# Optimization experiments

Measured on AMD Instinct MI355X. Metric: run time of the kernel, lower is better.

The kernel has to match this reference:

```python
import jax, jax.numpy as jnp
import numpy as np
from jax import lax

BN_EPS = 1e-5


def _fps(xyz, n_points):
    """Farthest point sampling. xyz: [B,N,3] -> [B,S] int32 indices.
    Sequential by nature; expressed as a lax.scan over S iterations.
    Deterministic start at index 0 (original uses a random start)."""
    B, N, _ = xyz.shape

    def step(carry, _):
        distance, farthest = carry  # [B,N], [B]
        centroid = jax.vmap(lambda p, f: p[f])(xyz, farthest)  # [B,3]
        dist = jnp.sum((xyz - centroid[:, None, :]) ** 2, axis=-1)  # [B,N]
        distance = jnp.minimum(distance, dist)
        new_far = jnp.argmax(distance, axis=-1).astype(jnp.int32)
        return (distance, new_far), farthest

    init = (jnp.full((B, N), 1e10, xyz.dtype), jnp.zeros((B,), jnp.int32))
    _, idxs = lax.scan(step, init, None, length=n_points)  # [S,B]
    return idxs.T  # [B,S]


def _gather(points, idx):
    """index_points: points [B,N,C], idx [B,...] -> [B,...,C]."""
    return jax.vmap(lambda p, i: p[i])(points, idx)


def _conv_bn_relu(x, W, b, gamma, beta):
    # 1x1 Conv2d over channel axis: x [B,Cin,k,S] -> [B,Cout,k,S]
    y = jnp.einsum('oc,bcks->boks', W, x) + b[None, :, None, None]
    # BatchNorm2d in training mode: batch stats over (B,k,S), biased variance
    m = jnp.mean(y, axis=(0, 2, 3), keepdims=True)
    v = jnp.var(y, axis=(0, 2, 3), keepdims=True)
    y = (y - m) * lax.rsqrt(v + BN_EPS) * gamma[None, :, None, None] + beta[None, :, None, None]
    return jax.nn.relu(y)


def setup_inputs() -> dict:
    key = jax.random.key(0)
    ks = jax.random.split(key, 4)
    B, N, D = 4, 16384, 125
    C0, C1, C2 = 128, 128, 256  # C0 = 3 + D
    xyz = jax.random.normal(ks[0], (B, N, 3), jnp.float32)
    features = jax.random.normal(ks[1], (B, N, D), jnp.float32)
    W1 = jax.random.normal(ks[2], (C1, C0), jnp.float32) / np.float32(np.sqrt(C0))
    W2 = jax.random.normal(ks[3], (C2, C1), jnp.float32) / np.float32(np.sqrt(C1))
    return {
        'xyz': xyz, 'features': features,
        'W1': W1, 'b1': jnp.zeros((C1,), jnp.float32),
        'gamma1': jnp.ones((C1,), jnp.float32), 'beta1': jnp.zeros((C1,), jnp.float32),
        'W2': W2, 'b2': jnp.zeros((C2,), jnp.float32),
        'gamma2': jnp.ones((C2,), jnp.float32), 'beta2': jnp.zeros((C2,), jnp.float32),
        'n_points_fps': 2048, 'k': 16,
    }


def reference(xyz, features, W1, b1, gamma1, beta1, W2, b2, gamma2, beta2, n_points_fps, k):
    B, N, _ = xyz.shape
    S = n_points_fps
    # sample_and_group
    fps_idx = _fps(xyz, S)                     # [B,S]
    new_xyz = _gather(xyz, fps_idx)            # [B,S,3]
    # full pairwise squared distances [B,S,N] (as in square_distance)
    dists = jnp.sum((new_xyz[:, :, None, :] - xyz[:, None, :, :]) ** 2, axis=-1)
    _, idx = lax.top_k(-dists, k)              # k nearest, ascending distance: [B,S,k]
    grouped_xyz = _gather(xyz, idx)            # [B,S,k,3]
    grouped_xyz_norm = grouped_xyz - new_xyz[:, :, None, :]
    grouped_feat = _gather(features, idx)      # [B,S,k,D]
    new_points = jnp.concatenate([grouped_xyz_norm, grouped_feat], axis=-1)  # [B,S,k,C0]
    # MLP head: permute to [B,C0,k,S]
    x = jnp.transpose(new_points, (0, 3, 2, 1))
    x = _conv_bn_relu(x, W1, b1, gamma1, beta1)
    x = _conv_bn_relu(x, W2, b2, gamma2, beta2)
    x = jnp.max(x, axis=2)                     # max over neighbors k: [B,C2,S]
    x = jnp.transpose(x, (0, 2, 1))            # [B,S,C2]
    return (new_xyz, x)
```

## Files before the change

### kernel.cpp

```cpp
#include <hip/hip_runtime.h>

#define B_ 4
#define N_ 16384
#define D_ 125
#define S_ 2048
#define K_ 16
#define C0_ 128
#define C1_ 128
#define C2_ 256
#define NSLOT 64

typedef float v2f __attribute__((ext_vector_type(2)));

__device__ __forceinline__ void pin(float& x) { asm volatile("" : "+v"(x)); }

__device__ __forceinline__ v2f v2max(v2f a, v2f b) {
  v2f r;
  r.x = fmaxf(a.x, b.x);
  r.y = fmaxf(a.y, b.y);
  return r;
}

template <int CTRL, int RMASK>
__device__ __forceinline__ double dppmax(double k) {
  const long long kb = __double_as_longlong(k);
  const int lo = (int)(kb & 0xffffffffll);
  const int hi = (int)(((unsigned long long)kb) >> 32);
  const int plo = __builtin_amdgcn_update_dpp(lo, lo, CTRL, RMASK, 0xf, false);
  const int phi = __builtin_amdgcn_update_dpp(hi, hi, CTRL, RMASK, 0xf, false);
  const double p =
      __longlong_as_double(((long long)phi << 32) | (unsigned int)plo);
  return fmax(k, p);
}
template <int CTRL, int RMASK>
__device__ __forceinline__ double dppmin(double k) {
  const long long kb = __double_as_longlong(k);
  const int lo = (int)(kb & 0xffffffffll);
  const int hi = (int)(((unsigned long long)kb) >> 32);
  const int plo = __builtin_amdgcn_update_dpp(lo, lo, CTRL, RMASK, 0xf, false);
  const int phi = __builtin_amdgcn_update_dpp(hi, hi, CTRL, RMASK, 0xf, false);
  const double p =
      __longlong_as_double(((long long)phi << 32) | (unsigned int)plo);
  return fmin(k, p);
}

__global__ __attribute__((amdgpu_flat_work_group_size(1024, 1024),
                          amdgpu_waves_per_eu(4, 4)))
void fps_kernel(const float* __restrict__ xyz, float* __restrict__ new_xyz,
                float* __restrict__ sortbuf) {
#pragma clang fp contract(off)
  const int b = blockIdx.x;
  const float* X = xyz + (size_t)b * N_ * 3;
  float* SB = sortbuf + (size_t)b * 3 * N_;
  const int t = threadIdx.x;
  constexpr int PAIRS = N_ / 1024 / 2;
  const int base = t * (2 * PAIRS);

  __shared__ unsigned int s_hist[4096];
  __shared__ float s_bb[16][8];
  __shared__ unsigned int s_wsum[16];
  __shared__ unsigned short s_sidx[N_];
  __shared__ unsigned long long s_k1[2];
  __shared__ __align__(16) float4 s_cc[2][16];

  float arr[48];
  {
    float4* a4 = (float4*)arr;
#pragma unroll
    for (int i = 0; i < 12; ++i) a4[i] = *(const float4*)(X + base * 3 + 4 * i);
  }
  float lx0 = arr[0], lx1 = arr[0], ly0 = arr[1], ly1 = arr[1];
  float lz0 = arr[2], lz1 = arr[2];
#pragma unroll
  for (int p = 1; p < 16; ++p) {
    lx0 = fminf(lx0, arr[3 * p + 0]); lx1 = fmaxf(lx1, arr[3 * p + 0]);
    ly0 = fminf(ly0, arr[3 * p + 1]); ly1 = fmaxf(ly1, arr[3 * p + 1]);
    lz0 = fminf(lz0, arr[3 * p + 2]); lz1 = fmaxf(lz1, arr[3 * p + 2]);
  }
#pragma unroll
  for (int off = 32; off > 0; off >>= 1) {
    lx0 = fminf(lx0, __shfl_xor(lx0, off)); lx1 = fmaxf(lx1, __shfl_xor(lx1, off));
    ly0 = fminf(ly0, __shfl_xor(ly0, off)); ly1 = fmaxf(ly1, __shfl_xor(ly1, off));
    lz0 = fminf(lz0, __shfl_xor(lz0, off)); lz1 = fmaxf(lz1, __shfl_xor(lz1, off));
  }
  if ((t & 63) == 0) {
    const int w = t >> 6;
    s_bb[w][0] = lx0; s_bb[w][1] = lx1; s_bb[w][2] = ly0;
    s_bb[w][3] = ly1; s_bb[w][4] = lz0; s_bb[w][5] = lz1;
  }
  for (int i = t; i < 4096; i += 1024) s_hist[i] = 0u;
  if (t == 0) { s_k1[0] = 0ull; s_k1[1] = 0ull; }
  __syncthreads();
  float gx0 = s_bb[0][0], gx1 = s_bb[0][1], gy0 = s_bb[0][2];
  float gy1 = s_bb[0][3], gz0 = s_bb[0][4], gz1 = s_bb[0][5];
#pragma unroll
  for (int w = 1; w < 16; ++w) {
    gx0 = fminf(gx0, s_bb[w][0]); gx1 = fmaxf(gx1, s_bb[w][1]);
    gy0 = fminf(gy0, s_bb[w][2]); gy1 = fmaxf(gy1, s_bb[w][3]);
    gz0 = fminf(gz0, s_bb[w][4]); gz1 = fmaxf(gz1, s_bb[w][5]);
  }
  const float ivx = (gx1 > gx0) ? 16.0f / (gx1 - gx0) : 0.0f;
  const float ivy = (gy1 > gy0) ? 16.0f / (gy1 - gy0) : 0.0f;
  const float ivz = (gz1 > gz0) ? 16.0f / (gz1 - gz0) : 0.0f;
  int cell[16];
#pragma unroll
  for (int p = 0; p < 16; ++p) {
    int qx = min(15, (int)((arr[3 * p + 0] - gx0) * ivx));
    int qy = min(15, (int)((arr[3 * p + 1] - gy0) * ivy));
    int qz = min(15, (int)((arr[3 * p + 2] - gz0) * ivz));
    int mx = (qx & 1) | ((qx & 2) << 2) | ((qx & 4) << 4) | ((qx & 8) << 6);
    int my = (qy & 1) | ((qy & 2) << 2) | ((qy & 4) << 4) | ((qy & 8) << 6);
    int mz = (qz & 1) | ((qz & 2) << 2) | ((qz & 4) << 4) | ((qz & 8) << 6);
    cell[p] = mx | (my << 1) | (mz << 2);
    atomicAdd(&s_hist[cell[p]], 1u);
  }
  __syncthreads();
  {
    unsigned int c0 = s_hist[4 * t + 0], c1 = s_hist[4 * t + 1];
    unsigned int c2 = s_hist[4 * t + 2], c3 = s_hist[4 * t + 3];
    (void)c3;
    unsigned int tsum = c0 + c1 + c2 + c3;
    unsigned int incl = tsum;
#pragma unroll
    for (int off = 1; off < 64; off <<= 1) {
      unsigned int nv = __shfl_up(incl, off);
      if ((t & 63) >= off) incl += nv;
    }
    if ((t & 63) == 63) s_wsum[t >> 6] = incl;
    __syncthreads();
    unsigned int wpre = 0;
    const int myw = t >> 6;
    for (int w = 0; w < myw; ++w) wpre += s_wsum[w];
    const unsigned int texc = wpre + incl - tsum;
    s_hist[4 * t + 0] = texc;
    s_hist[4 * t + 1] = texc + c0;
    s_hist[4 * t + 2] = texc + c0 + c1;
    s_hist[4 * t + 3] = texc + c0 + c1 + c2;
  }
  __syncthreads();
#pragma unroll
  for (int p = 0; p < 16; ++p) {
    const unsigned int slot = atomicAdd(&s_hist[cell[p]], 1u);
    SB[slot]          = arr[3 * p + 0];
    SB[N_ + slot]     = arr[3 * p + 1];
    SB[2 * N_ + slot] = arr[3 * p + 2];
    s_sidx[slot] = (unsigned short)(base + p);
  }
  __threadfence();
  __syncthreads();
  __threadfence();

  v2f px[PAIRS], py[PAIRS], pz[PAIRS], d[PAIRS];
  {
    float4 xa[4], ya[4], za[4];
#pragma unroll
    for (int i = 0; i < 4; ++i) {
      xa[i] = *(const float4*)(SB + base + 4 * i);
      ya[i] = *(const float4*)(SB + N_ + base + 4 * i);
      za[i] = *(const float4*)(SB + 2 * N_ + base + 4 * i);
    }
    const float* xf = (const float*)xa;
    const float* yf = (const float*)ya;
    const float* zf = (const float*)za;
#pragma unroll
    for (int j = 0; j < PAIRS; ++j) {
      px[j] = (v2f){xf[2 * j], xf[2 * j + 1]};
      py[j] = (v2f){yf[2 * j], yf[2 * j + 1]};
      pz[j] = (v2f){zf[2 * j], zf[2 * j + 1]};
      d[j] = (v2f){1e10f, 1e10f};
    }
  }
  unsigned int invw[PAIRS];
  {
    const unsigned int* SI = (const unsigned int*)&s_sidx[base];
#pragma unroll
    for (int j = 0; j < PAIRS; ++j) invw[j] = ~SI[j];
  }
  float bx0 = 1e30f, bx1 = -1e30f, by0 = 1e30f, by1 = -1e30f;
  float bz0 = 1e30f, bz1 = -1e30f;
#pragma unroll
  for (int j = 0; j < PAIRS; ++j) {
    bx0 = fminf(bx0, fminf(px[j].x, px[j].y));
    bx1 = fmaxf(bx1, fmaxf(px[j].x, px[j].y));
    by0 = fminf(by0, fminf(py[j].x, py[j].y));
    by1 = fmaxf(by1, fmaxf(py[j].x, py[j].y));
    bz0 = fminf(bz0, fminf(pz[j].x, pz[j].y));
    bz1 = fmaxf(bz1, fmaxf(pz[j].x, pz[j].y));
  }
#pragma unroll
  for (int j = 0; j < PAIRS; ++j) {
    float a0 = px[j].x, a1 = px[j].y;
    float b0 = py[j].x, b1 = py[j].y;
    float c0 = pz[j].x, c1 = pz[j].y;
    pin(a0); pin(a1); pin(b0); pin(b1); pin(c0); pin(c1);
    px[j] = (v2f){a0, a1};
    py[j] = (v2f){b0, b1};
    pz[j] = (v2f){c0, c1};
  }
  float cx = X[0], cy = X[1], cz = X[2];
  float tmax = 1e10f;
  unsigned long long keylow = 0ull;
  bool iwin = false;
  float ccx = 0.f, ccy = 0.f, ccz = 0.f;
  float cap_x = 0.f, cap_y = 0.f, cap_z = 0.f;
  const unsigned int wid = (unsigned int)(t >> 6);
  for (int s = 0; s < S_; ++s) {
    if (((s - t) & 1023) == 0) { cap_x = cx; cap_y = cy; cap_z = cz; }
    if ((s & 1023) == 1023) {
      const int o = (b * S_ + (s & ~1023) + t) * 3;
      new_xyz[o + 0] = cap_x;
      new_xyz[o + 1] = cap_y;
      new_xyz[o + 2] = cap_z;
    }
    if (s == S_ - 1) break;
    const int buf = s & 1;
    const float mx = fmaxf(fmaxf(bx0 - cx, cx - bx1), 0.0f);
    const float my = fmaxf(fmaxf(by0 - cy, cy - by1), 0.0f);
    const float mz = fmaxf(fmaxf(bz0 - cz, cz - bz1), 0.0f);
    const float L = (mx * mx + my * my) + mz * mz;
    if (__any(L < tmax)) {
      __builtin_amdgcn_s_setprio(1);
      const v2f c2x = {cx, cx}, c2y = {cy, cy}, c2z = {cz, cz};
#pragma unroll
      for (int j = 0; j < PAIRS; ++j) {
        v2f dx = px[j] - c2x;
        v2f dy = py[j] - c2y;
        v2f dz = pz[j] - c2z;
        v2f sq = (dx * dx + dy * dy) + dz * dz;
        v2f dm;
        dm.x = fminf(d[j].x, sq.x);
        dm.y = fminf(d[j].y, sq.y);
        d[j] = dm;
      }
      const v2f m01 = v2max(d[0], d[1]);
      const v2f m23 = v2max(d[2], d[3]);
      const v2f m45 = v2max(d[4], d[5]);
      const v2f m67 = v2max(d[6], d[7]);
      const v2f m03 = v2max(m01, m23);
      const v2f m47 = v2max(m45, m67);
      const v2f m07 = v2max(m03, m47);
      const float lmax = fmaxf(m07.x, m07.y);
      tmax = lmax;
      unsigned int binv = 0u;
#pragma unroll
      for (int j = 0; j < PAIRS; ++j) {
        const unsigned int lo = invw[j] & 0xFFFFu;
        const unsigned int hi = invw[j] >> 16;
        if (d[j].x == lmax) binv = max(binv, lo);
        if (d[j].y == lmax) binv = max(binv, hi);
      }
#pragma unroll
      for (int j = 0; j < PAIRS; ++j) {
        const unsigned int lo = invw[j] & 0xFFFFu;
        const unsigned int hi = invw[j] >> 16;
        if (lo == binv) { ccx = px[j].x; ccy = py[j].x; ccz = pz[j].x; }
        if (hi == binv) { ccx = px[j].y; ccy = py[j].y; ccz = pz[j].y; }
      }
      const unsigned long long k52 =
          ((unsigned long long)__float_as_uint(lmax) << 20) |
          (unsigned long long)((binv << 4) | wid);
      double dk = __longlong_as_double((long long)k52);
      dk = dppmax<0x111, 0xf>(dk);
      dk = dppmax<0x112, 0xf>(dk);
      dk = dppmax<0x114, 0xf>(dk);
      dk = dppmax<0x118, 0xf>(dk);
      dk = dppmax<0x142, 0xa>(dk);
      dk = dppmax<0x143, 0xc>(dk);
      const long long kb = __double_as_longlong(dk);
      const int rlo = __builtin_amdgcn_readlane((int)(kb & 0xffffffffll), 63);
      const int rhi =
          __builtin_amdgcn_readlane((int)(((unsigned long long)kb) >> 32), 63);
      const unsigned long long wk52 =
          ((unsigned long long)(unsigned int)rhi << 32) | (unsigned int)rlo;
      iwin = (k52 == wk52);
      keylow = wk52;
      __builtin_amdgcn_s_setprio(0);
    }
    if (iwin) {
      atomicMax(&s_k1[buf], ((unsigned long long)s << 52) | keylow);
      s_cc[buf][wid] = make_float4(ccx, ccy, ccz, 0.f);
    }
    __syncthreads();
    const unsigned long long bk = s_k1[buf];
    const int w_win = (int)(bk & 15ull);
    const float4 cc = s_cc[buf][w_win];
    cx = cc.x; cy = cc.y; cz = cc.z;
  }
}

__global__ __launch_bounds__(256) void knn_kernel(const float* __restrict__ xyz,
                                                  const float* __restrict__ new_xyz,
                                                  int* __restrict__ knn_idx) {
  const int q = blockIdx.x;
  const int b = q / S_;
  __shared__ float sd[N_];
  __shared__ unsigned long long s_kd[2];
  const int t = threadIdx.x;
  if (t == 0) { s_kd[0] = ~0ull; s_kd[1] = ~0ull; }
  const float qx = new_xyz[q * 3 + 0];
  const float qy = new_xyz[q * 3 + 1];
  const float qz = new_xyz[q * 3 + 2];
  const float* X = xyz + (size_t)b * N_ * 3;
  float lmin = 1e30f;
  int lidx = -1;
  for (int j = 0; j < N_ / 256; ++j) {
    int i = t + j * 256;
    float dx = X[i * 3 + 0] - qx;
    float dy = X[i * 3 + 1] - qy;
    float dz = X[i * 3 + 2] - qz;
    float dsq = fmaf(dx, dx, fmaf(dy, dy, dz * dz));
    sd[i] = dsq;
    if (dsq < lmin) { lmin = dsq; lidx = i; }
  }
  __syncthreads();
  for (int r = 0; r < K_; ++r) {
    const unsigned long long k =
        ((unsigned long long)(7 - (r >> 1)) << 60) |
        ((unsigned long long)__float_as_uint(lmin) << 28) |
        (unsigned int)(lidx & 0x0FFFFFFF);
    double dk = __longlong_as_double((long long)k);
    dk = dppmin<0x111, 0xf>(dk);
    dk = dppmin<0x112, 0xf>(dk);
    dk = dppmin<0x114, 0xf>(dk);
    dk = dppmin<0x118, 0xf>(dk);
    dk = dppmin<0x142, 0xa>(dk);
    dk = dppmin<0x143, 0xc>(dk);
    const long long kb = __double_as_longlong(dk);
    const int rlo = __builtin_amdgcn_readlane((int)(kb & 0xffffffffll), 63);
    const int rhi =
        __builtin_amdgcn_readlane((int)(((unsigned long long)kb) >> 32), 63);
    const unsigned long long wk =
        ((unsigned long long)(unsigned int)rhi << 32) | (unsigned int)rlo;
    if ((t & 63) == 0) atomicMin(&s_kd[r & 1], wk);
    __syncthreads();
    const unsigned long long bk = s_kd[r & 1];
    const int wi = (int)(bk & 0x0FFFFFFFull);
    if (t == 0) knn_idx[q * K_ + r] = wi;
    if (wi == lidx) {
      sd[wi] = 1e30f;
      lmin = 1e30f; lidx = -1;
      for (int j = 0; j < N_ / 256; ++j) {
        int i = t + j * 256;
        float dv = sd[i];
        if (dv < lmin) { lmin = dv; lidx = i; }
      }
    }
  }
}

__global__ __launch_bounds__(256) void prep_kernel(const float* __restrict__ W1,
                                                   const float* __restrict__ W2,
                                                   float* __restrict__ W1t,
                                                   float* __restrict__ W2t,
                                                   float* __restrict__ stats) {
  int e = blockIdx.x * 256 + threadIdx.x;
  stats[e] = 0.0f;
  if (e < C1_ * C0_) {
    int co = e / C0_, c = e % C0_;
    W1t[c * C1_ + co] = W1[e];
  } else {
    int e2 = e - C1_ * C0_;
    int co = e2 / C1_, c = e2 % C1_;
    W2t[c * C2_ + co] = W2[e2];
  }
}

__global__ __launch_bounds__(256) void conv1_stats_kernel(
    const float* __restrict__ xyz, const float* __restrict__ feat,
    const float* __restrict__ new_xyz, const int* __restrict__ knn,
    const float* __restrict__ W1t, const float* __restrict__ b1,
    float* __restrict__ stats1) {
  __shared__ __align__(16) float sinT[C0_][K_];
  __shared__ int sidx[K_];
  __shared__ float sred[256];
  const int t = threadIdx.x;
  float psum = 0.f, psumsq = 0.f;
  const int QPB = (B_ * S_) / 1024;
  for (int qq = 0; qq < QPB; ++qq) {
    const int q = blockIdx.x * QPB + qq;
    const int b = q / S_;
    if (t < K_) sidx[t] = knn[q * K_ + t];
    __syncthreads();
    const float nx = new_xyz[q * 3 + 0];
    const float ny = new_xyz[q * 3 + 1];
    const float nz = new_xyz[q * 3 + 2];
    for (int e = t; e < K_ * C0_; e += 256) {
      int c = e >> 4, kk = e & 15;
      int i = sidx[kk];
      float v;
      if (c < 3)
        v = xyz[((size_t)b * N_ + i) * 3 + c] - (c == 0 ? nx : (c == 1 ? ny : nz));
      else
        v = feat[((size_t)b * N_ + i) * D_ + (c - 3)];
      sinT[c][kk] = v;
    }
    __syncthreads();
    const int co = t & 127, kh = t >> 7;
    float acc[8];
    float bias = b1[co];
#pragma unroll
    for (int k = 0; k < 8; ++k) acc[k] = bias;
    for (int c = 0; c < C0_; ++c) {
      float w = W1t[c * C1_ + co];
      float4 xa = *(const float4*)&sinT[c][kh * 8];
      float4 xb = *(const float4*)&sinT[c][kh * 8 + 4];
      acc[0] = fmaf(w, xa.x, acc[0]);
      acc[1] = fmaf(w, xa.y, acc[1]);
      acc[2] = fmaf(w, xa.z, acc[2]);
      acc[3] = fmaf(w, xa.w, acc[3]);
      acc[4] = fmaf(w, xb.x, acc[4]);
      acc[5] = fmaf(w, xb.y, acc[5]);
      acc[6] = fmaf(w, xb.z, acc[6]);
      acc[7] = fmaf(w, xb.w, acc[7]);
    }
#pragma unroll
    for (int k = 0; k < 8; ++k) {
      psum += acc[k];
      psumsq = fmaf(acc[k], acc[k], psumsq);
    }
    __syncthreads();
  }
  sred[t] = psum;
  __syncthreads();
  float totsum = (t < 128) ? (sred[t] + sred[t + 128]) : 0.f;
  __syncthreads();
  sred[t] = psumsq;
  __syncthreads();
  if (t < 128) {
    float totsq = sred[t] + sred[t + 128];
    float* st = stats1 + (size_t)(blockIdx.x & (NSLOT - 1)) * (2 * C1_);
    atomicAdd(&st[t], totsum);
    atomicAdd(&st[C1_ + t], totsq);
  }
}

__global__ void finalize1_kernel(const float* __restrict__ stats1,
                                 const float* __restrict__ gamma1,
                                 const float* __restrict__ beta1,
                                 float* __restrict__ ss1) {
  int t = threadIdx.x;
  float s = 0.f, sq = 0.f;
  for (int w = 0; w < NSLOT; ++w) {
    s += stats1[w * 2 * C1_ + t];
    sq += stats1[w * 2 * C1_ + C1_ + t];
  }
  const float M = (float)(B_ * S_ * K_);
  float m = s / M;
  float v = fmaxf(sq / M - m * m, 0.f);
  float sc = gamma1[t] * rsqrtf(v + 1e-5f);
  ss1[t] = sc;
  ss1[C1_ + t] = fmaf(-m, sc, beta1[t]);
}

__global__ __launch_bounds__(256) void conv2_kernel(
    const float* __restrict__ xyz, const float* __restrict__ feat,
    const float* __restrict__ new_xyz, const int* __restrict__ knn,
    const float* __restrict__ W1t, const float* __restrict__ b1,
    const float* __restrict__ ss1, const float* __restrict__ W2t,
    const float* __restrict__ b2, float* __restrict__ maxv,
    float* __restrict__ minv, float* __restrict__ stats2) {
  __shared__ __align__(16) float sinT[C0_][K_];
  __shared__ __align__(16) float sh1T[C1_][20];
  __shared__ int sidx[K_];
  const int t = threadIdx.x;
  float psum = 0.f, psumsq = 0.f;
  const int QPB = (B_ * S_) / 1024;
  for (int qq = 0; qq < QPB; ++qq) {
    const int q = blockIdx.x * QPB + qq;
    const int b = q / S_;
    if (t < K_) sidx[t] = knn[q * K_ + t];
    __syncthreads();
    const float nx = new_xyz[q * 3 + 0];
    const float ny = new_xyz[q * 3 + 1];
    const float nz = new_xyz[q * 3 + 2];
    for (int e = t; e < K_ * C0_; e += 256) {
      int c = e >> 4, kk = e & 15;
      int i = sidx[kk];
      float v;
      if (c < 3)
        v = xyz[((size_t)b * N_ + i) * 3 + c] - (c == 0 ? nx : (c == 1 ? ny : nz));
      else
        v = feat[((size_t)b * N_ + i) * D_ + (c - 3)];
      sinT[c][kk] = v;
    }
    __syncthreads();
    {
      const int co = t & 127, kh = t >> 7;
      float acc[8];
      float bias = b1[co];
#pragma unroll
      for (int k = 0; k < 8; ++k) acc[k] = bias;
      for (int c = 0; c < C0_; ++c) {
        float w = W1t[c * C1_ + co];
        float4 xa = *(const float4*)&sinT[c][kh * 8];
        float4 xb = *(const float4*)&sinT[c][kh * 8 + 4];
        acc[0] = fmaf(w, xa.x, acc[0]);
        acc[1] = fmaf(w, xa.y, acc[1]);
        acc[2] = fmaf(w, xa.z, acc[2]);
        acc[3] = fmaf(w, xa.w, acc[3]);
        acc[4] = fmaf(w, xb.x, acc[4]);
        acc[5] = fmaf(w, xb.y, acc[5]);
        acc[6] = fmaf(w, xb.z, acc[6]);
        acc[7] = fmaf(w, xb.w, acc[7]);
      }
      float sc = ss1[co], sh = ss1[C1_ + co];
#pragma unroll
      for (int k = 0; k < 8; ++k) {
        float h = fmaxf(fmaf(acc[k], sc, sh), 0.f);
        sh1T[co][kh * 8 + k] = h;
      }
    }
    __syncthreads();
    {
      float acc2[16];
      float bias2 = b2[t];
#pragma unroll
      for (int k = 0; k < 16; ++k) acc2[k] = bias2;
      for (int c = 0; c < C1_; ++c) {
        float w = W2t[c * C2_ + t];
        float4 h0 = *(const float4*)&sh1T[c][0];
        float4 h1 = *(const float4*)&sh1T[c][4];
        float4 h2 = *(const float4*)&sh1T[c][8];
        float4 h3 = *(const float4*)&sh1T[c][12];
        acc2[0] = fmaf(w, h0.x, acc2[0]);
        acc2[1] = fmaf(w, h0.y, acc2[1]);
        acc2[2] = fmaf(w, h0.z, acc2[2]);
        acc2[3] = fmaf(w, h0.w, acc2[3]);
        acc2[4] = fmaf(w, h1.x, acc2[4]);
        acc2[5] = fmaf(w, h1.y, acc2[5]);
        acc2[6] = fmaf(w, h1.z, acc2[6]);
        acc2[7] = fmaf(w, h1.w, acc2[7]);
        acc2[8] = fmaf(w, h2.x, acc2[8]);
        acc2[9] = fmaf(w, h2.y, acc2[9]);
        acc2[10] = fmaf(w, h2.z, acc2[10]);
        acc2[11] = fmaf(w, h2.w, acc2[11]);
        acc2[12] = fmaf(w, h3.x, acc2[12]);
        acc2[13] = fmaf(w, h3.y, acc2[13]);
        acc2[14] = fmaf(w, h3.z, acc2[14]);
        acc2[15] = fmaf(w, h3.w, acc2[15]);
      }
      float mx = acc2[0], mn = acc2[0];
#pragma unroll
      for (int k = 0; k < 16; ++k) {
        psum += acc2[k];
        psumsq = fmaf(acc2[k], acc2[k], psumsq);
        mx = fmaxf(mx, acc2[k]);
        mn = fminf(mn, acc2[k]);
      }
      maxv[(size_t)q * C2_ + t] = mx;
      minv[(size_t)q * C2_ + t] = mn;
    }
    __syncthreads();
  }
  float* st = stats2 + (size_t)(blockIdx.x & (NSLOT - 1)) * (2 * C2_);
  atomicAdd(&st[t], psum);
  atomicAdd(&st[C2_ + t], psumsq);
}

__global__ void finalize2_kernel(const float* __restrict__ stats2,
                                 const float* __restrict__ gamma2,
                                 const float* __restrict__ beta2,
                                 float* __restrict__ ss2) {
  int t = threadIdx.x;
  float s = 0.f, sq = 0.f;
  for (int w = 0; w < NSLOT; ++w) {
    s += stats2[w * 2 * C2_ + t];
    sq += stats2[w * 2 * C2_ + C2_ + t];
  }
  const float M = (float)(B_ * S_ * K_);
  float m = s / M;
  float v = fmaxf(sq / M - m * m, 0.f);
  float sc = gamma2[t] * rsqrtf(v + 1e-5f);
  ss2[t] = sc;
  ss2[C2_ + t] = fmaf(-m, sc, beta2[t]);
}

__global__ __launch_bounds__(256) void out_kernel(const float* __restrict__ maxv,
                                                  const float* __restrict__ minv,
                                                  const float* __restrict__ ss2,
                                                  float* __restrict__ out2) {
  int e = blockIdx.x * 256 + threadIdx.x;
  int co = e & (C2_ - 1);
  float sc = ss2[co], sh = ss2[C2_ + co];
  float v = (sc >= 0.f) ? maxv[e] : minv[e];
  out2[e] = fmaxf(fmaf(v, sc, sh), 0.f);
}

extern "C" void kernel_launch(void* const* d_in, const int* in_sizes, int n_in,
                              void* d_out, int out_size, void* d_ws, size_t ws_size,
                              hipStream_t stream) {
  (void)in_sizes; (void)n_in; (void)out_size; (void)ws_size;
  const float* xyz = (const float*)d_in[0];
  const float* feat = (const float*)d_in[1];
  const float* W1 = (const float*)d_in[2];
  const float* b1 = (const float*)d_in[3];
  const float* gamma1 = (const float*)d_in[4];
  const float* beta1 = (const float*)d_in[5];
  const float* W2 = (const float*)d_in[6];
  const float* b2 = (const float*)d_in[7];
  const float* gamma2 = (const float*)d_in[8];
  const float* beta2 = (const float*)d_in[9];

  float* out = (float*)d_out;
  float* new_xyz = out;
  float* out2 = out + B_ * S_ * 3;

  float* ws = (float*)d_ws;
  float* stats1 = ws;
  float* stats2 = stats1 + NSLOT * 2 * C1_;
  float* ss1 = stats2 + NSLOT * 2 * C2_;
  float* ss2 = ss1 + 2 * C1_;
  float* W1t = ss2 + 2 * C2_;
  float* W2t = W1t + C1_ * C0_;
  int* knn = (int*)(W2t + (size_t)C2_ * C1_);
  float* maxv = (float*)(knn + B_ * S_ * K_);
  float* minv = maxv + (size_t)B_ * S_ * C2_;
  float* sortbuf = maxv;

  prep_kernel<<<192, 256, 0, stream>>>(W1, W2, W1t, W2t, stats1);
  fps_kernel<<<B_, 1024, 0, stream>>>(xyz, new_xyz, sortbuf);
  knn_kernel<<<B_ * S_, 256, 0, stream>>>(xyz, new_xyz, knn);
  conv1_stats_kernel<<<1024, 256, 0, stream>>>(xyz, feat, new_xyz, knn, W1t, b1, stats1);
  finalize1_kernel<<<1, 128, 0, stream>>>(stats1, gamma1, beta1, ss1);
  conv2_kernel<<<1024, 256, 0, stream>>>(xyz, feat, new_xyz, knn, W1t, b1, ss1,
                                         W2t, b2, maxv, minv, stats2);
  finalize2_kernel<<<1, 256, 0, stream>>>(stats2, gamma2, beta2, ss2);
  out_kernel<<<(B_ * S_ * C2_) / 256, 256, 0, stream>>>(maxv, minv, ss2, out2);
}
```

Measured before the change: 3.317 ms.

## Split FPS in two halves and overlap second half with KNN of first half

FPS is split into two kernels. The first computes the first 1024 samples and spills its per-thread state (distances, index words, centroid, keys) to workspace. A fused kernel then resumes FPS for the remaining samples in 4 blocks while the other blocks run KNN on the already-written first-half centroids, and a final kernel runs KNN for the second half. KNN blocks also grow from 256 to 1024 threads. This hides the serial FPS tail behind KNN work, at the cost of spilling and reloading state and sharing CUs between the serial FPS blocks and KNN blocks.

```diff
diff --git a/kernel.cpp b/kernel.cpp
--- a/kernel.cpp
+++ b/kernel.cpp
@@ -46,8 +46,11 @@
 
 __global__ __attribute__((amdgpu_flat_work_group_size(1024, 1024),
                           amdgpu_waves_per_eu(4, 4)))
-void fps_kernel(const float* __restrict__ xyz, float* __restrict__ new_xyz,
-                float* __restrict__ sortbuf) {
+void fps_a_kernel(const float* __restrict__ xyz, float* __restrict__ new_xyz,
+                  float* __restrict__ sortbuf, float* __restrict__ dsp,
+                  float4* __restrict__ ccsp, unsigned int* __restrict__ invsp,
+                  unsigned long long* __restrict__ klsp,
+                  float4* __restrict__ csp) {
 #pragma clang fp contract(off)
   const int b = blockIdx.x;
   const float* X = xyz + (size_t)b * N_ * 3;
@@ -204,7 +207,7 @@
   float ccx = 0.f, ccy = 0.f, ccz = 0.f;
   float cap_x = 0.f, cap_y = 0.f, cap_z = 0.f;
   const unsigned int wid = (unsigned int)(t >> 6);
-  for (int s = 0; s < S_; ++s) {
+  for (int s = 0; s < 1024; ++s) {
     if (((s - t) & 1023) == 0) { cap_x = cx; cap_y = cy; cap_z = cz; }
     if ((s & 1023) == 1023) {
       const int o = (b * S_ + (s & ~1023) + t) * 3;
@@ -212,7 +215,6 @@
       new_xyz[o + 1] = cap_y;
       new_xyz[o + 2] = cap_z;
     }
-    if (s == S_ - 1) break;
     const int buf = s & 1;
     const float mx = fmaxf(fmaxf(bx0 - cx, cx - bx1), 0.0f);
     const float my = fmaxf(fmaxf(by0 - cy, cy - by1), 0.0f);
@@ -286,15 +288,203 @@
     const float4 cc = s_cc[buf][w_win];
     cx = cc.x; cy = cc.y; cz = cc.z;
   }
-}
-
-__global__ __launch_bounds__(256) void knn_kernel(const float* __restrict__ xyz,
-                                                  const float* __restrict__ new_xyz,
-                                                  int* __restrict__ knn_idx) {
-  const int q = blockIdx.x;
-  const int b = q / S_;
-  __shared__ float sd[N_];
-  __shared__ unsigned long long s_kd[2];
+  {
+    float4* o = (float4*)(dsp + ((size_t)b * 1024 + t) * 16);
+    o[0] = make_float4(d[0].x, d[0].y, d[1].x, d[1].y);
+    o[1] = make_float4(d[2].x, d[2].y, d[3].x, d[3].y);
+    o[2] = make_float4(d[4].x, d[4].y, d[5].x, d[5].y);
+    o[3] = make_float4(d[6].x, d[6].y, d[7].x, d[7].y);
+    ccsp[b * 1024 + t] = make_float4(ccx, ccy, ccz, iwin ? 1.f : 0.f);
+    unsigned int* iv = invsp + ((size_t)b * 1024 + t) * 8;
+#pragma unroll
+    for (int j = 0; j < PAIRS; ++j) iv[j] = invw[j];
+    if ((t & 63) == 0) klsp[b * 16 + wid] = keylow;
+    if (t == 0) csp[b] = make_float4(cx, cy, cz, 0.f);
+  }
+}
+
+__device__ void fps_b_body(const float* __restrict__ xyz,
+                           float* __restrict__ new_xyz,
+                           float* __restrict__ sortbuf,
+                           float* __restrict__ dsp, float4* __restrict__ ccsp,
+                           unsigned int* __restrict__ invsp,
+                           unsigned long long* __restrict__ klsp,
+                           float4* __restrict__ csp, char* smem) {
+#pragma clang fp contract(off)
+  const int b = blockIdx.x;
+  const float* X = xyz + (size_t)b * N_ * 3;
+  float* SB = sortbuf + (size_t)b * 3 * N_;
+  const int t = threadIdx.x;
+  constexpr int PAIRS = N_ / 1024 / 2;
+  const int base = t * (2 * PAIRS);
+  unsigned long long* s_k1 = (unsigned long long*)smem;
+  float4* s_cc = (float4*)(smem + 32);
+  (void)X;
+
+  v2f px[PAIRS], py[PAIRS], pz[PAIRS], d[PAIRS];
+  {
+    float4 xa[4], ya[4], za[4];
+#pragma unroll
+    for (int i = 0; i < 4; ++i) {
+      xa[i] = *(const float4*)(SB + base + 4 * i);
+      ya[i] = *(const float4*)(SB + N_ + base + 4 * i);
+      za[i] = *(const float4*)(SB + 2 * N_ + base + 4 * i);
+    }
+    const float* xf = (const float*)xa;
+    const float* yf = (const float*)ya;
+    const float* zf = (const float*)za;
+#pragma unroll
+    for (int j = 0; j < PAIRS; ++j) {
+      px[j] = (v2f){xf[2 * j], xf[2 * j + 1]};
+      py[j] = (v2f){yf[2 * j], yf[2 * j + 1]};
+      pz[j] = (v2f){zf[2 * j], zf[2 * j + 1]};
+    }
+  }
+  {
+    const float4* i4 = (const float4*)(dsp + ((size_t)b * 1024 + t) * 16);
+    float4 d0 = i4[0], d1 = i4[1], d2 = i4[2], d3 = i4[3];
+    d[0] = (v2f){d0.x, d0.y}; d[1] = (v2f){d0.z, d0.w};
+    d[2] = (v2f){d1.x, d1.y}; d[3] = (v2f){d1.z, d1.w};
+    d[4] = (v2f){d2.x, d2.y}; d[5] = (v2f){d2.z, d2.w};
+    d[6] = (v2f){d3.x, d3.y}; d[7] = (v2f){d3.z, d3.w};
+  }
+  unsigned int invw[PAIRS];
+  {
+    const unsigned int* iv = invsp + ((size_t)b * 1024 + t) * 8;
+#pragma unroll
+    for (int j = 0; j < PAIRS; ++j) invw[j] = iv[j];
+  }
+  const float4 ccv = ccsp[b * 1024 + t];
+  float ccx = ccv.x, ccy = ccv.y, ccz = ccv.z;
+  bool iwin = (ccv.w != 0.f);
+  const unsigned int wid = (unsigned int)(t >> 6);
+  unsigned long long keylow = klsp[b * 16 + wid];
+  const float4 cv = csp[b];
+  float cx = cv.x, cy = cv.y, cz = cv.z;
+  float tmax;
+  {
+    const v2f m01 = v2max(d[0], d[1]);
+    const v2f m23 = v2max(d[2], d[3]);
+    const v2f m45 = v2max(d[4], d[5]);
+    const v2f m67 = v2max(d[6], d[7]);
+    const v2f m03 = v2max(m01, m23);
+    const v2f m47 = v2max(m45, m67);
+    const v2f m07 = v2max(m03, m47);
+    tmax = fmaxf(m07.x, m07.y);
+  }
+  float bx0 = 1e30f, bx1 = -1e30f, by0 = 1e30f, by1 = -1e30f;
+  float bz0 = 1e30f, bz1 = -1e30f;
+#pragma unroll
+  for (int j = 0; j < PAIRS; ++j) {
+    bx0 = fminf(bx0, fminf(px[j].x, px[j].y));
+    bx1 = fmaxf(bx1, fmaxf(px[j].x, px[j].y));
+    by0 = fminf(by0, fminf(py[j].x, py[j].y));
+    by1 = fmaxf(by1, fmaxf(py[j].x, py[j].y));
+    bz0 = fminf(bz0, fminf(pz[j].x, pz[j].y));
+    bz1 = fmaxf(bz1, fmaxf(pz[j].x, pz[j].y));
+  }
+#pragma unroll
+  for (int j = 0; j < PAIRS; ++j) {
+    float a0 = px[j].x, a1 = px[j].y;
+    float b0 = py[j].x, b1 = py[j].y;
+    float c0 = pz[j].x, c1 = pz[j].y;
+    pin(a0); pin(a1); pin(b0); pin(b1); pin(c0); pin(c1);
+    px[j] = (v2f){a0, a1};
+    py[j] = (v2f){b0, b1};
+    pz[j] = (v2f){c0, c1};
+  }
+  if (t == 0) { s_k1[0] = 0ull; s_k1[1] = 0ull; }
+  __syncthreads();
+  float cap_x = 0.f, cap_y = 0.f, cap_z = 0.f;
+  for (int s = 1024; s < S_; ++s) {
+    if (((s - t) & 1023) == 0) { cap_x = cx; cap_y = cy; cap_z = cz; }
+    if ((s & 1023) == 1023) {
+      const int o = (b * S_ + (s & ~1023) + t) * 3;
+      new_xyz[o + 0] = cap_x;
+      new_xyz[o + 1] = cap_y;
+      new_xyz[o + 2] = cap_z;
+    }
+    if (s == S_ - 1) break;
+    const int buf = s & 1;
+    const float mx = fmaxf(fmaxf(bx0 - cx, cx - bx1), 0.0f);
+    const float my = fmaxf(fmaxf(by0 - cy, cy - by1), 0.0f);
+    const float mz = fmaxf(fmaxf(bz0 - cz, cz - bz1), 0.0f);
+    const float L = (mx * mx + my * my) + mz * mz;
+    if (__any(L < tmax)) {
+      __builtin_amdgcn_s_setprio(1);
+      const v2f c2x = {cx, cx}, c2y = {cy, cy}, c2z = {cz, cz};
+#pragma unroll
+      for (int j = 0; j < PAIRS; ++j) {
+        v2f dx = px[j] - c2x;
+        v2f dy = py[j] - c2y;
+        v2f dz = pz[j] - c2z;
+        v2f sq = (dx * dx + dy * dy) + dz * dz;
+        v2f dm;
+        dm.x = fminf(d[j].x, sq.x);
+        dm.y = fminf(d[j].y, sq.y);
+        d[j] = dm;
+      }
+      const v2f m01 = v2max(d[0], d[1]);
+      const v2f m23 = v2max(d[2], d[3]);
+      const v2f m45 = v2max(d[4], d[5]);
+      const v2f m67 = v2max(d[6], d[7]);
+      const v2f m03 = v2max(m01, m23);
+      const v2f m47 = v2max(m45, m67);
+      const v2f m07 = v2max(m03, m47);
+      const float lmax = fmaxf(m07.x, m07.y);
+      tmax = lmax;
+      unsigned int binv = 0u;
+#pragma unroll
+      for (int j = 0; j < PAIRS; ++j) {
+        const unsigned int lo = invw[j] & 0xFFFFu;
+        const unsigned int hi = invw[j] >> 16;
+        if (d[j].x == lmax) binv = max(binv, lo);
+        if (d[j].y == lmax) binv = max(binv, hi);
+      }
+#pragma unroll
+      for (int j = 0; j < PAIRS; ++j) {
+        const unsigned int lo = invw[j] & 0xFFFFu;
+        const unsigned int hi = invw[j] >> 16;
+        if (lo == binv) { ccx = px[j].x; ccy = py[j].x; ccz = pz[j].x; }
+        if (hi == binv) { ccx = px[j].y; ccy = py[j].y; ccz = pz[j].y; }
+      }
+      const unsigned long long k52 =
+          ((unsigned long long)__float_as_uint(lmax) << 20) |
+          (unsigned long long)((binv << 4) | wid);
+      double dk = __longlong_as_double((long long)k52);
+      dk = dppmax<0x111, 0xf>(dk);
+      dk = dppmax<0x112, 0xf>(dk);
+      dk = dppmax<0x114, 0xf>(dk);
+      dk = dppmax<0x118, 0xf>(dk);
+      dk = dppmax<0x142, 0xa>(dk);
+      dk = dppmax<0x143, 0xc>(dk);
+      const long long kb = __double_as_longlong(dk);
+      const int rlo = __builtin_amdgcn_readlane((int)(kb & 0xffffffffll), 63);
+      const int rhi =
+          __builtin_amdgcn_readlane((int)(((unsigned long long)kb) >> 32), 63);
+      const unsigned long long wk52 =
+          ((unsigned long long)(unsigned int)rhi << 32) | (unsigned int)rlo;
+      iwin = (k52 == wk52);
+      keylow = wk52;
+      __builtin_amdgcn_s_setprio(0);
+    }
+    if (iwin) {
+      atomicMax(&s_k1[buf], ((unsigned long long)s << 52) | keylow);
+      s_cc[buf * 16 + wid] = make_float4(ccx, ccy, ccz, 0.f);
+    }
+    __syncthreads();
+    const unsigned long long bk = s_k1[buf];
+    const int w_win = (int)(bk & 15ull);
+    const float4 cc = s_cc[buf * 16 + w_win];
+    cx = cc.x; cy = cc.y; cz = cc.z;
+  }
+}
+
+__device__ __forceinline__ void knn_core(float* sd, unsigned long long* s_kd,
+                                         const float* __restrict__ xyz,
+                                         const float* __restrict__ new_xyz,
+                                         int* __restrict__ knn_idx, int q,
+                                         int b) {
   const int t = threadIdx.x;
   if (t == 0) { s_kd[0] = ~0ull; s_kd[1] = ~0ull; }
   const float qx = new_xyz[q * 3 + 0];
@@ -303,8 +493,8 @@
   const float* X = xyz + (size_t)b * N_ * 3;
   float lmin = 1e30f;
   int lidx = -1;
-  for (int j = 0; j < N_ / 256; ++j) {
-    int i = t + j * 256;
+  for (int j = 0; j < N_ / 1024; ++j) {
+    int i = t + j * 1024;
     float dx = X[i * 3 + 0] - qx;
     float dy = X[i * 3 + 1] - qy;
     float dz = X[i * 3 + 2] - qz;
@@ -339,13 +529,43 @@
     if (wi == lidx) {
       sd[wi] = 1e30f;
       lmin = 1e30f; lidx = -1;
-      for (int j = 0; j < N_ / 256; ++j) {
-        int i = t + j * 256;
+      for (int j = 0; j < N_ / 1024; ++j) {
+        int i = t + j * 1024;
         float dv = sd[i];
         if (dv < lmin) { lmin = dv; lidx = i; }
       }
     }
   }
+}
+
+__global__ __attribute__((amdgpu_flat_work_group_size(1024, 1024),
+                          amdgpu_waves_per_eu(4, 4)))
+void fused_b_kernel(const float* __restrict__ xyz, float* __restrict__ new_xyz,
+                    float* __restrict__ sortbuf, float* __restrict__ dsp,
+                    float4* __restrict__ ccsp, unsigned int* __restrict__ invsp,
+                    unsigned long long* __restrict__ klsp,
+                    float4* __restrict__ csp, int* __restrict__ knn_idx) {
+  __shared__ __align__(16) char smem[N_ * 4 + 16];
+  if (blockIdx.x >= B_) {
+    const int idx = blockIdx.x - B_;
+    const int b = idx >> 10;
+    const int s = idx & 1023;
+    knn_core((float*)smem, (unsigned long long*)(smem + N_ * 4), xyz, new_xyz,
+             knn_idx, b * S_ + s, b);
+    return;
+  }
+  fps_b_body(xyz, new_xyz, sortbuf, dsp, ccsp, invsp, klsp, csp, smem);
+}
+
+__global__ __attribute__((amdgpu_flat_work_group_size(1024, 1024)))
+void knn2_kernel(const float* __restrict__ xyz,
+                 const float* __restrict__ new_xyz, int* __restrict__ knn_idx) {
+  __shared__ float sd[N_];
+  __shared__ unsigned long long s_kd[2];
+  const int idx = blockIdx.x;
+  const int b = idx >> 10;
+  const int s = 1024 + (idx & 1023);
+  knn_core(sd, s_kd, xyz, new_xyz, knn_idx, b * S_ + s, b);
 }
 
 __global__ __launch_bounds__(256) void prep_kernel(const float* __restrict__ W1,
@@ -616,10 +836,19 @@
   float* maxv = (float*)(knn + B_ * S_ * K_);
   float* minv = maxv + (size_t)B_ * S_ * C2_;
   float* sortbuf = maxv;
+  float* dsp = minv;
+  float4* ccsp = (float4*)(minv + 65536);
+  unsigned int* invsp = (unsigned int*)(minv + 65536 + 16384);
+  unsigned long long* klsp =
+      (unsigned long long*)(minv + 65536 + 16384 + 32768);
+  float4* csp = (float4*)(minv + 65536 + 16384 + 32768 + 2 * B_ * 16);
 
   prep_kernel<<<192, 256, 0, stream>>>(W1, W2, W1t, W2t, stats1);
-  fps_kernel<<<B_, 1024, 0, stream>>>(xyz, new_xyz, sortbuf);
-  knn_kernel<<<B_ * S_, 256, 0, stream>>>(xyz, new_xyz, knn);
+  fps_a_kernel<<<B_, 1024, 0, stream>>>(xyz, new_xyz, sortbuf, dsp, ccsp,
+                                        invsp, klsp, csp);
+  fused_b_kernel<<<B_ + B_ * 1024, 1024, 0, stream>>>(
+      xyz, new_xyz, sortbuf, dsp, ccsp, invsp, klsp, csp, knn);
+  knn2_kernel<<<B_ * 1024, 1024, 0, stream>>>(xyz, new_xyz, knn);
   conv1_stats_kernel<<<1024, 256, 0, stream>>>(xyz, feat, new_xyz, knn, W1t, b1, stats1);
   finalize1_kernel<<<1, 128, 0, stream>>>(stats1, gamma1, beta1, ss1);
   conv2_kernel<<<1024, 256, 0, stream>>>(xyz, feat, new_xyz, knn, W1t, b1, ss1,
```

Result: faster. 3.166 ms (-4.5%).
